# Performance work log

Hardware: AMD Instinct MI355X
Metric: run time of the kernel (lower is better)

The kernel has to match this reference:

```python
import jax, jax.numpy as jnp
import numpy as np

TOPK = 8            # args.topk
SWAP_RATIO = 0.3    # args.swap_ratio
NUM_SPECIAL = 999   # first non-special wordpiece id in bert-base-uncased


def setup_inputs() -> dict:
    key = jax.random.key(0)
    k0, k1, k2, k3, k4, k5 = jax.random.split(key, 6)
    B, S, V, D = 4, 512, 30522, 768
    return {
        "delta_grad": jax.random.normal(k0, (B, S, D), jnp.float32),
        "src_embeds": jax.random.normal(k1, (B, S, D), jnp.float32),
        "embedding_matrix": jax.random.normal(k2, (V, D), jnp.float32),
        "src_tokens": jax.random.randint(k3, (B, S), 0, V),
        "pred_lm": jax.random.normal(k4, (B, S, V), jnp.float32),
        "attention_mask": jnp.ones((B, S), jnp.int32),
        "rand_u": jax.random.uniform(k5, (B, S), jnp.float32),
    }


def reference(delta_grad, src_embeds, embedding_matrix, src_tokens, pred_lm, attention_mask, rand_u):
    B, S, D = delta_grad.shape
    V = embedding_matrix.shape[0]
    neg_inf = jnp.float32(-np.inf)

    # dir_dot_grad = -(prev_dot - new_dot) = new_dot - prev_dot
    new_dot = jnp.einsum('bsd,vd->bsv', delta_grad, embedding_matrix)   # [B,S,V]
    prev_dot = jnp.einsum('bsd,bsd->bs', delta_grad, src_embeds)        # [B,S]
    dir_dot_grad = new_dot - prev_dot[..., None]

    # pairwise euclidean distance between src_embeds and vocab embeddings
    src_sq = jnp.sum(src_embeds * src_embeds, axis=-1)                  # [B,S]
    vocab_sq = jnp.sum(embedding_matrix * embedding_matrix, axis=-1)    # [V]
    dot = jnp.einsum('bsd,vd->bsv', src_embeds, embedding_matrix)       # [B,S,V]
    sq_norm = src_sq[..., None] + vocab_sq[None, None, :] - 2.0 * dot
    dir_norm = jnp.sqrt(jax.nn.relu(sq_norm) + 1e-20)

    dir_dot_grad = dir_dot_grad / dir_norm

    # LM top-k allowed-token mask (scatter of 0 into a -inf mask in torch)
    _, topk_idx = jax.lax.top_k(pred_lm, TOPK)                          # [B,S,K]
    topk_idx = topk_idx * attention_mask[..., None].astype(topk_idx.dtype)
    bi = jnp.arange(B)[:, None, None]
    si = jnp.arange(S)[None, :, None]
    allowed = jnp.zeros((B, S, V), bool).at[bi, si, topk_idx].set(True)

    filtered = jnp.where(allowed, dir_dot_grad, neg_inf)
    # special tokens [:999] -> -inf (overrides any topk scatter there)
    filtered = jnp.where(jnp.arange(V)[None, None, :] < NUM_SPECIAL, neg_inf, filtered)
    # forbid keeping the original token
    filtered = jnp.where(jnp.arange(V)[None, None, :] == src_tokens[..., None], neg_inf, filtered)

    adv_flip = jnp.argmax(filtered, axis=2)                             # [B,S]

    # swap mask: non-special positions, Bernoulli(swap_ratio)
    no_special = src_tokens >= NUM_SPECIAL
    swap = rand_u > (1.0 - SWAP_RATIO)
    mask_idx = (no_special & swap).astype(src_tokens.dtype)

    adv_tokens = src_tokens * (1 - mask_idx) + adv_flip.astype(src_tokens.dtype) * mask_idx
    return adv_tokens
```

## Files before the change

kernel.cpp:

```cpp
#include <hip/hip_runtime.h>
#include <math.h>
#include <float.h>

constexpr int TOPK = 8;
constexpr int NUM_SPECIAL = 999;
constexpr int V = 30522;
constexpr int D = 768;
constexpr int BLOCK = 256;
constexpr int V2 = V / 2;
constexpr int CAP = 512;

__device__ __forceinline__ unsigned long long fkey(float v, unsigned int idx) {
    unsigned int u = __float_as_uint(v);
    u = ((int)u < 0) ? ~u : (u | 0x80000000u);
    return ((unsigned long long)u << 32) | (unsigned long long)(~idx);
}

__global__ __launch_bounds__(BLOCK) void dvat_kernel(
    const float* __restrict__ delta_grad,
    const float* __restrict__ src_embeds,
    const float* __restrict__ emb,
    const int*   __restrict__ src_tokens,
    const float* __restrict__ pred_lm,
    const int*   __restrict__ attn,
    const float* __restrict__ rand_u,
    int* __restrict__ out)
{
    const int pos = blockIdx.x;
    const int tid = threadIdx.x;
    const int lane = tid & 63;
    const int wave = tid >> 6;

    __shared__ float sh_vals[BLOCK * TOPK];
    __shared__ unsigned long long sh_cand64[CAP];
    __shared__ int    s_ncand;
    __shared__ float  s_g8;
    __shared__ int    s_cand[TOPK];
    __shared__ double s_scores[TOPK];
    __shared__ double s_pd[4], s_ssq[4];

    const float2* row2 = (const float2*)(pred_lm + (size_t)pos * V);

    float vx[TOPK], vy[TOPK];
    #pragma unroll
    for (int j = 0; j < TOPK; ++j) { vx[j] = -INFINITY; vy[j] = -INFINITY; }

    for (int i = tid; i < V2; i += BLOCK) {
        float2 f = row2[i];
        float t = f.x;
        #pragma unroll
        for (int j = 0; j < TOPK; ++j) {
            float m = fmaxf(vx[j], t); t = fminf(vx[j], t); vx[j] = m;
        }
        t = f.y;
        #pragma unroll
        for (int j = 0; j < TOPK; ++j) {
            float m = fmaxf(vy[j], t); t = fminf(vy[j], t); vy[j] = m;
        }
    }
    float v8[TOPK];
    #pragma unroll
    for (int j = 0; j < TOPK; ++j) v8[j] = fmaxf(vx[j], vy[TOPK - 1 - j]);

    #pragma unroll
    for (int j = 0; j < TOPK; ++j) sh_vals[j * BLOCK + tid] = v8[j];
    __syncthreads();

    for (int it = 0; it < TOPK; ++it) {
        if (tid < 64) {
            float m = -INFINITY; int ms = 0;
            for (int j = tid; j < BLOCK * TOPK; j += 64) {
                float x = sh_vals[j];
                if (x > m) { m = x; ms = j; }
            }
            #pragma unroll
            for (int off = 32; off; off >>= 1) {
                float om = __shfl_down(m, off, 64);
                int   os = __shfl_down(ms, off, 64);
                if (om > m) { m = om; ms = os; }
            }
            if (tid == 0) {
                sh_vals[ms] = -INFINITY;
                if (it == TOPK - 1) s_g8 = m;
            }
        }
        __syncthreads();
    }

    if (tid == 0) s_ncand = 0;
    __syncthreads();
    const float g8 = s_g8;
    for (int i = tid; i < V2; i += BLOCK) {
        float2 f = row2[i];
        if (f.x >= g8) {
            int p = atomicAdd(&s_ncand, 1);
            if (p < CAP) sh_cand64[p] = fkey(f.x, (unsigned)(2 * i));
        }
        if (f.y >= g8) {
            int p = atomicAdd(&s_ncand, 1);
            if (p < CAP) sh_cand64[p] = fkey(f.y, (unsigned)(2 * i + 1));
        }
    }
    __syncthreads();
    const int ncand = min(s_ncand, CAP);

    for (int it = 0; it < TOPK; ++it) {
        if (tid < 64) {
            unsigned long long m = 0ull; int ms = 0;
            for (int j = tid; j < ncand; j += 64) {
                unsigned long long x = sh_cand64[j];
                if (x > m) { m = x; ms = j; }
            }
            #pragma unroll
            for (int off = 32; off; off >>= 1) {
                unsigned long long om = __shfl_down(m, off, 64);
                int os = __shfl_down(ms, off, 64);
                if (om > m) { m = om; ms = os; }
            }
            if (tid == 0) {
                s_cand[it] = (m == 0ull) ? 0 : (int)(~(unsigned int)m);
                sh_cand64[ms] = 0ull;
            }
        }
        __syncthreads();
    }

    if (tid == 0 && attn[pos] == 0) {
        #pragma unroll
        for (int k = 0; k < TOPK; ++k) s_cand[k] = 0;
    }
    __syncthreads();

    float* shf = sh_vals;
    const float* dg = delta_grad + (size_t)pos * D;
    const float* se = src_embeds + (size_t)pos * D;

    double pd = 0.0, ssq = 0.0;
    for (int i = tid; i < D; i += BLOCK) {
        float g = dg[i], e = se[i];
        shf[i] = g;
        shf[D + i] = e;
        pd  += (double)g * (double)e;
        ssq += (double)e * (double)e;
    }
    #pragma unroll
    for (int off = 32; off; off >>= 1) {
        pd  += __shfl_down(pd, off, 64);
        ssq += __shfl_down(ssq, off, 64);
    }
    if (lane == 0) { s_pd[wave] = pd; s_ssq[wave] = ssq; }
    __syncthreads();

    const double prev_dot = s_pd[0] + s_pd[1] + s_pd[2] + s_pd[3];
    const double src_sq   = s_ssq[0] + s_ssq[1] + s_ssq[2] + s_ssq[3];

    #pragma unroll
    for (int kk = 0; kk < 2; ++kk) {
        const int k = 2 * wave + kk;
        const int v = s_cand[k];
        const float* ev = emb + (size_t)v * D;
        double ddg = 0.0, dse = 0.0, dvv = 0.0;
        for (int i = lane; i < D; i += 64) {
            double e = (double)ev[i];
            ddg += e * (double)shf[i];
            dse += e * (double)shf[D + i];
            dvv += e * e;
        }
        #pragma unroll
        for (int off = 32; off; off >>= 1) {
            ddg += __shfl_down(ddg, off, 64);
            dse += __shfl_down(dse, off, 64);
            dvv += __shfl_down(dvv, off, 64);
        }
        if (lane == 0) {
            double sq = src_sq + dvv - 2.0 * dse;
            if (sq < 0.0) sq = 0.0;
            double dn = sqrt(sq + 1e-20);
            s_scores[k] = (ddg - prev_dot) / dn;
        }
    }
    __syncthreads();

    if (tid == 0) {
        const int src_tok = src_tokens[pos];
        int best = 0;
        double best_s = 0.0;
        bool found = false;
        #pragma unroll
        for (int k = 0; k < TOPK; ++k) {
            const int v = s_cand[k];
            if (v < NUM_SPECIAL || v == src_tok) continue;
            const double sc = s_scores[k];
            if (!found || sc > best_s || (sc == best_s && v < best)) {
                best = v; best_s = sc; found = true;
            }
        }
        const int adv_flip = found ? best : 0;
        const bool no_special = (src_tok >= NUM_SPECIAL);
        const bool swap = (rand_u[pos] > 0.7f);
        out[pos] = (no_special && swap) ? adv_flip : src_tok;
    }
}

extern "C" void kernel_launch(void* const* d_in, const int* in_sizes, int n_in,
                              void* d_out, int out_size, void* d_ws, size_t ws_size,
                              hipStream_t stream) {
    const float* delta_grad = (const float*)d_in[0];
    const float* src_embeds = (const float*)d_in[1];
    const float* emb        = (const float*)d_in[2];
    const int*   src_tokens = (const int*)d_in[3];
    const float* pred_lm    = (const float*)d_in[4];
    const int*   attn       = (const int*)d_in[5];
    const float* randu      = (const float*)d_in[6];
    int* out = (int*)d_out;

    const int BS = in_sizes[3];
    dvat_kernel<<<BS, BLOCK, 0, stream>>>(delta_grad, src_embeds, emb,
                                          src_tokens, pred_lm, attn, randu, out);
}
```

Baseline: 457.5 us.

## Replace serial top-8 merge with wave shuffles and rescan only hot threads

The serialized 8-pass shared-memory reduction for the 8th-largest value is replaced by a per-thread bitonic sort, a wave-level shuffle extraction and a single-wave final merge. The second pass over the pred_lm row now revisits only the strided slices owned by threads whose local max reached the threshold, with a fallback full scan when too many threads qualify. The main loop is also unrolled 4x with loads issued together, and the launch bounds request 8 blocks per CU. The aim is to cut the syncthreads-heavy merge and roughly halve global reads of the 122KB row, at the cost of more code and extra index arithmetic.

```diff
diff --git a/kernel.cpp b/kernel.cpp
--- a/kernel.cpp
+++ b/kernel.cpp
@@ -1,6 +1,5 @@
 #include <hip/hip_runtime.h>
 #include <math.h>
-#include <float.h>
 
 constexpr int TOPK = 8;
 constexpr int NUM_SPECIAL = 999;
@@ -8,7 +7,10 @@
 constexpr int D = 768;
 constexpr int BLOCK = 256;
 constexpr int V2 = V / 2;
+constexpr int NQ = 14;
+constexpr int NK = (V2 + BLOCK - 1) / BLOCK;
 constexpr int CAP = 512;
+constexpr int HOTCAP = 64;
 
 __device__ __forceinline__ unsigned long long fkey(float v, unsigned int idx) {
     unsigned int u = __float_as_uint(v);
@@ -16,7 +18,44 @@
     return ((unsigned long long)u << 32) | (unsigned long long)(~idx);
 }
 
-__global__ __launch_bounds__(BLOCK) void dvat_kernel(
+__device__ __forceinline__ void net8(float (&L)[TOPK], float t) {
+    #pragma unroll
+    for (int j = 0; j < TOPK; ++j) {
+        float m = fmaxf(L[j], t); t = fminf(L[j], t); L[j] = m;
+    }
+}
+
+__device__ __forceinline__ void cmpx(float& a, float& b) {
+    float m = fmaxf(a, b), n = fminf(a, b); a = m; b = n;
+}
+__device__ __forceinline__ void bitonic_sort8_desc(float (&v)[TOPK]) {
+    cmpx(v[0], v[4]); cmpx(v[1], v[5]); cmpx(v[2], v[6]); cmpx(v[3], v[7]);
+    cmpx(v[0], v[2]); cmpx(v[1], v[3]); cmpx(v[4], v[6]); cmpx(v[5], v[7]);
+    cmpx(v[0], v[1]); cmpx(v[2], v[3]); cmpx(v[4], v[5]); cmpx(v[6], v[7]);
+}
+
+__device__ __forceinline__ void wave_extract8(float (&cur)[TOPK], int lane,
+                                              float* dst) {
+    #pragma unroll
+    for (int r = 0; r < TOPK; ++r) {
+        float m = cur[0];
+        int ml = lane;
+        #pragma unroll
+        for (int off = 1; off < 64; off <<= 1) {
+            float om = __shfl_xor(m, off, 64);
+            int   ol = __shfl_xor(ml, off, 64);
+            if (om > m || (om == m && ol < ml)) { m = om; ml = ol; }
+        }
+        if (lane == ml) {
+            #pragma unroll
+            for (int j = 0; j < TOPK - 1; ++j) cur[j] = cur[j + 1];
+            cur[TOPK - 1] = -INFINITY;
+        }
+        if (lane == 0) dst[r] = m;
+    }
+}
+
+__global__ __launch_bounds__(BLOCK, 8) void dvat_kernel(
     const float* __restrict__ delta_grad,
     const float* __restrict__ src_embeds,
     const float* __restrict__ emb,
@@ -31,13 +70,18 @@
     const int lane = tid & 63;
     const int wave = tid >> 6;
 
-    __shared__ float sh_vals[BLOCK * TOPK];
+    __shared__ float  sm32[32];
+    __shared__ float  s_g8;
+    __shared__ int    s_hot[HOTCAP];
+    __shared__ int    s_nhot;
+    __shared__ int    s_ncand;
     __shared__ unsigned long long sh_cand64[CAP];
-    __shared__ int    s_ncand;
-    __shared__ float  s_g8;
     __shared__ int    s_cand[TOPK];
     __shared__ double s_scores[TOPK];
     __shared__ double s_pd[4], s_ssq[4];
+    __shared__ float  shf[2 * D];
+
+    if (tid == 0) { s_nhot = 0; s_ncand = 0; }
 
     const float2* row2 = (const float2*)(pred_lm + (size_t)pos * V);
 
@@ -45,60 +89,86 @@
     #pragma unroll
     for (int j = 0; j < TOPK; ++j) { vx[j] = -INFINITY; vy[j] = -INFINITY; }
 
-    for (int i = tid; i < V2; i += BLOCK) {
+    int i = tid;
+    for (int q = 0; q < NQ; ++q, i += 4 * BLOCK) {
+        float2 a = row2[i];
+        float2 b = row2[i + BLOCK];
+        float2 c = row2[i + 2 * BLOCK];
+        float2 d = row2[i + 3 * BLOCK];
+        net8(vx, a.x); net8(vy, a.y);
+        net8(vx, b.x); net8(vy, b.y);
+        net8(vx, c.x); net8(vy, c.y);
+        net8(vx, d.x); net8(vy, d.y);
+    }
+    for (; i < V2; i += BLOCK) {
         float2 f = row2[i];
-        float t = f.x;
-        #pragma unroll
-        for (int j = 0; j < TOPK; ++j) {
-            float m = fmaxf(vx[j], t); t = fminf(vx[j], t); vx[j] = m;
-        }
-        t = f.y;
-        #pragma unroll
-        for (int j = 0; j < TOPK; ++j) {
-            float m = fmaxf(vy[j], t); t = fminf(vy[j], t); vy[j] = m;
-        }
-    }
+        net8(vx, f.x); net8(vy, f.y);
+    }
+
     float v8[TOPK];
     #pragma unroll
     for (int j = 0; j < TOPK; ++j) v8[j] = fmaxf(vx[j], vy[TOPK - 1 - j]);
-
-    #pragma unroll
-    for (int j = 0; j < TOPK; ++j) sh_vals[j * BLOCK + tid] = v8[j];
-    __syncthreads();
-
-    for (int it = 0; it < TOPK; ++it) {
-        if (tid < 64) {
-            float m = -INFINITY; int ms = 0;
-            for (int j = tid; j < BLOCK * TOPK; j += 64) {
-                float x = sh_vals[j];
-                if (x > m) { m = x; ms = j; }
-            }
+    bitonic_sort8_desc(v8);
+    const float tmax = v8[0];
+
+    wave_extract8(v8, lane, &sm32[wave * 8]);
+    __syncthreads();
+
+    if (wave == 0) {
+        float c = (lane < 32) ? sm32[lane] : -INFINITY;
+        float m = -INFINITY;
+        #pragma unroll
+        for (int r = 0; r < TOPK; ++r) {
+            m = c; int ml = lane;
             #pragma unroll
-            for (int off = 32; off; off >>= 1) {
-                float om = __shfl_down(m, off, 64);
-                int   os = __shfl_down(ms, off, 64);
-                if (om > m) { m = om; ms = os; }
-            }
-            if (tid == 0) {
-                sh_vals[ms] = -INFINITY;
-                if (it == TOPK - 1) s_g8 = m;
-            }
-        }
-        __syncthreads();
-    }
-
-    if (tid == 0) s_ncand = 0;
+            for (int off = 1; off < 64; off <<= 1) {
+                float om = __shfl_xor(m, off, 64);
+                int   ol = __shfl_xor(ml, off, 64);
+                if (om > m || (om == m && ol < ml)) { m = om; ml = ol; }
+            }
+            if (lane == ml) c = -INFINITY;
+        }
+        if (lane == 0) s_g8 = m;
+    }
     __syncthreads();
     const float g8 = s_g8;
-    for (int i = tid; i < V2; i += BLOCK) {
-        float2 f = row2[i];
-        if (f.x >= g8) {
-            int p = atomicAdd(&s_ncand, 1);
-            if (p < CAP) sh_cand64[p] = fkey(f.x, (unsigned)(2 * i));
-        }
-        if (f.y >= g8) {
-            int p = atomicAdd(&s_ncand, 1);
-            if (p < CAP) sh_cand64[p] = fkey(f.y, (unsigned)(2 * i + 1));
+
+    if (tmax >= g8) {
+        int p = atomicAdd(&s_nhot, 1);
+        if (p < HOTCAP) s_hot[p] = tid;
+    }
+    __syncthreads();
+
+    if (s_nhot <= HOTCAP) {
+        const int nhot = s_nhot;
+        const int total = nhot * NK;
+        for (int w = tid; w < total; w += BLOCK) {
+            const int h = w / NK;
+            const int k = w - h * NK;
+            const int i2 = s_hot[h] + (k << 8);
+            if (i2 < V2) {
+                float2 f = row2[i2];
+                if (f.x >= g8) {
+                    int p = atomicAdd(&s_ncand, 1);
+                    if (p < CAP) sh_cand64[p] = fkey(f.x, (unsigned)(2 * i2));
+                }
+                if (f.y >= g8) {
+                    int p = atomicAdd(&s_ncand, 1);
+                    if (p < CAP) sh_cand64[p] = fkey(f.y, (unsigned)(2 * i2 + 1));
+                }
+            }
+        }
+    } else {
+        for (int i2 = tid; i2 < V2; i2 += BLOCK) {
+            float2 f = row2[i2];
+            if (f.x >= g8) {
+                int p = atomicAdd(&s_ncand, 1);
+                if (p < CAP) sh_cand64[p] = fkey(f.x, (unsigned)(2 * i2));
+            }
+            if (f.y >= g8) {
+                int p = atomicAdd(&s_ncand, 1);
+                if (p < CAP) sh_cand64[p] = fkey(f.y, (unsigned)(2 * i2 + 1));
+            }
         }
     }
     __syncthreads();
@@ -131,15 +201,14 @@
     }
     __syncthreads();
 
-    float* shf = sh_vals;
     const float* dg = delta_grad + (size_t)pos * D;
     const float* se = src_embeds + (size_t)pos * D;
 
     double pd = 0.0, ssq = 0.0;
-    for (int i = tid; i < D; i += BLOCK) {
-        float g = dg[i], e = se[i];
-        shf[i] = g;
-        shf[D + i] = e;
+    for (int ii = tid; ii < D; ii += BLOCK) {
+        float g = dg[ii], e = se[ii];
+        shf[ii] = g;
+        shf[D + ii] = e;
         pd  += (double)g * (double)e;
         ssq += (double)e * (double)e;
     }
@@ -160,10 +229,10 @@
         const int v = s_cand[k];
         const float* ev = emb + (size_t)v * D;
         double ddg = 0.0, dse = 0.0, dvv = 0.0;
-        for (int i = lane; i < D; i += 64) {
-            double e = (double)ev[i];
-            ddg += e * (double)shf[i];
-            dse += e * (double)shf[D + i];
+        for (int ii = lane; ii < D; ii += 64) {
+            double e = (double)ev[ii];
+            ddg += e * (double)shf[ii];
+            dse += e * (double)shf[D + ii];
             dvv += e * e;
         }
         #pragma unroll
```

New measurement: 414.0 us. 9.5% less time.
